# Performance work log

Hardware: AMD Instinct MI355X
Metric: run time of the kernel (lower is better)

The kernel has to match this reference:

```python
import jax, jax.numpy as jnp
import numpy as np


def setup_inputs() -> dict:
    key = jax.random.key(0)
    k1, k2 = jax.random.split(key)
    B, T, D, K = 16, 1024, 256, 8192
    x = jax.random.normal(k1, (B, T, D), dtype=jnp.float32)
    # mimic nn.Embedding init uniform_(-1/K, 1/K)
    codebook = jax.random.uniform(k2, (K, D), dtype=jnp.float32,
                                  minval=-1.0 / K, maxval=1.0 / K)
    return {"x": x, "codebook": codebook}


def reference(x, codebook):
    sg = jax.lax.stop_gradient
    x2 = jnp.sum(x * x, axis=-1, keepdims=True)               # [B, T, 1]
    c2 = jnp.sum(codebook * codebook, axis=-1)                # [K]
    xc = jnp.einsum('btd,kd->btk', x, codebook)               # [B, T, K]
    dist2 = x2 - 2.0 * xc + c2                                # [B, T, K]
    indices = jnp.argmin(dist2, axis=-1)                      # [B, T] int
    cb_vecs = codebook[indices]                               # [B, T, D]
    # straight-through estimator
    quantized = x + sg(cb_vecs - x)
    codebook_loss = jnp.mean((quantized - sg(x)) ** 2)
    commitment_loss = jnp.mean((sg(quantized) - x) ** 2)
    quantize_loss = codebook_loss + commitment_loss
    return (quantized, indices, quantize_loss)
```

## Files before the change

### kernel.cpp

```cpp
#include <hip/hip_runtime.h>
#include <float.h>

typedef __attribute__((ext_vector_type(8))) short short8;
typedef __attribute__((ext_vector_type(4))) float f32x4;

#define BT    16384
#define DM    256
#define KC    8192
#define QOFF  (BT * DM)
#define LOFF  (QOFF + BT)
#define MARGIN 2e-4f

#define E_XH 0
#define E_CH (BT * DM)
#define WS_BF16_BYTES ((size_t)(BT * DM + KC * DM) * 2)
#define WS_SLOT_OFF   WS_BF16_BYTES
#define WS_SLOT_BYTES ((size_t)64 * BT * 8)
#define WS_LP_OFF     (WS_SLOT_OFF + WS_SLOT_BYTES)
#define WS_NEED       (WS_LP_OFF + 4096 * 4)


__device__ inline ushort bf16rne(float f) {
    unsigned u = __float_as_uint(f);
    return (ushort)((u + 0x7FFFu + ((u >> 16) & 1u)) >> 16);
}
__device__ inline unsigned umax2(unsigned a, unsigned b) { return a > b ? a : b; }
__device__ inline unsigned umin2(unsigned a, unsigned b) { return a < b ? a : b; }

__device__ __forceinline__ void gl_lds16(const void* g, void* l) {
    __builtin_amdgcn_global_load_lds(
        (const __attribute__((address_space(1))) void*)g,
        (__attribute__((address_space(3))) void*)l, 16, 0, 0);
}

__global__ __launch_bounds__(256) void k_cvt(const float* __restrict__ x,
                                             const float* __restrict__ cb,
                                             ushort* __restrict__ ws) {
    const int XN = BT * DM / 4;
    const int CN = KC * DM / 4;
    int idx = blockIdx.x * 256 + threadIdx.x;
    const float4* src;
    ushort* dh; int o;
    if (idx < XN) { src = (const float4*)x; dh = ws + E_XH; o = idx; }
    else {
        o = idx - XN;
        if (o >= CN) return;
        src = (const float4*)cb; dh = ws + E_CH;
    }
    float4 v = src[o];
    ushort4 h;
    h.x = bf16rne(v.x);
    h.y = bf16rne(v.y);
    h.z = bf16rne(v.z);
    h.w = bf16rne(v.w);
    ((ushort4*)dh)[o] = h;
}

__global__ __launch_bounds__(512, 4) void k_main_mfma(const ushort* __restrict__ ws,
                                                      uint2* __restrict__ slotb) {
    __shared__ ushort sTok[2][64 * 256];
    __shared__ uint2  msc[2][4][64];

    const int tid = threadIdx.x;
    const int w = tid >> 6, L = tid & 63;
    const int lq = L >> 4, lr = L & 15;
    const int wm = w >> 1, wn = w & 1;
    const int grp   = blockIdx.x >> 3;
    const int chunk = blockIdx.x & 7;
    const int c0    = grp * 128 + wm * 32;
    const int tok0  = chunk * 2048;
    const unsigned lw = ((unsigned)wm << 5) | ((unsigned)lq << 2);

    const short8* ch8 = (const short8*)(ws + E_CH);
    const uint4*  xh4 = (const uint4*)(ws + E_XH);

    short8 a[2][8];
    #pragma unroll
    for (int i = 0; i < 2; ++i)
        #pragma unroll
        for (int ks = 0; ks < 8; ++ks)
            a[i][ks] = ch8[(size_t)(c0 + i * 16 + lr) * 32 + ks * 4 + lq];

    const int half = L >> 5;
    const int g32  = L & 31;

    {
        const uint4* src = xh4 + (size_t)(tok0 + w * 8) * 32;
        #pragma unroll
        for (int q = 0; q < 4; ++q) {
            int rrel = 2 * q + half;
            gl_lds16(src + (size_t)rrel * 32 + (g32 ^ (rrel & 7)),
                     &sTok[0][(w * 8 + 2 * q) * 256]);
        }
    }
    __syncthreads();

    uint2 mb0, mb1, mb2, mb3;

    auto emit = [&](uint2 mv, int pp) {
        slotb[(size_t)grp * BT + tok0 + pp * 64 + L] = mv;
    };

    for (int t = 0; t < 8; ++t) {
        #pragma unroll
        for (int pi = 0; pi < 4; ++pi) {
            const int p   = t * 4 + pi;
            const int cur = pi & 1;

            if (t < 7 || pi < 3) {
                const uint4* src = xh4 + (size_t)(tok0 + (p + 1) * 64 + w * 8) * 32;
                #pragma unroll
                for (int q = 0; q < 4; ++q) {
                    int rrel = 2 * q + half;
                    gl_lds16(src + (size_t)rrel * 32 + (g32 ^ (rrel & 7)),
                             &sTok[cur ^ 1][(w * 8 + 2 * q) * 256]);
                }
            }

            f32x4 acc[2][2];
            #pragma unroll
            for (int i = 0; i < 2; ++i)
                #pragma unroll
                for (int j = 0; j < 2; ++j)
                    acc[i][j] = (f32x4){0.25f, 0.25f, 0.25f, 0.25f};

            const ushort* tb = &sTok[cur][0];
            __builtin_amdgcn_s_setprio(1);
            #pragma unroll
            for (int ks = 0; ks < 8; ++ks) {
                short8 b[2];
                #pragma unroll
                for (int j = 0; j < 2; ++j) {
                    int row = wn * 32 + j * 16 + lr;
                    b[j] = *(const short8*)(tb + row * 256 + (((ks * 4 + lq) ^ (lr & 7)) * 8));
                }
                #pragma unroll
                for (int i = 0; i < 2; ++i)
                    #pragma unroll
                    for (int j = 0; j < 2; ++j)
                        acc[i][j] = __builtin_amdgcn_mfma_f32_16x16x32_bf16(a[i][ks], b[j], acc[i][j], 0, 0, 0);
            }
            __builtin_amdgcn_s_setprio(0);

            #pragma unroll
            for (int j = 0; j < 2; ++j) {
                unsigned h[4], l[4];
                #pragma unroll
                for (int i = 0; i < 2; ++i)
                    #pragma unroll
                    for (int rp = 0; rp < 2; ++rp) {
                        unsigned e0 = (__float_as_uint(acc[i][j][2 * rp])     & 0xFFFFFF80u) | lw | (i << 4) | (2 * rp);
                        unsigned e1 = (__float_as_uint(acc[i][j][2 * rp + 1]) & 0xFFFFFF80u) | lw | (i << 4) | (2 * rp + 1);
                        h[i * 2 + rp] = umax2(e0, e1);
                        l[i * 2 + rp] = umin2(e0, e1);
                    }
                unsigned ha = umax2(h[0], h[2]);
                unsigned la = umax2(umin2(h[0], h[2]), umax2(l[0], l[2]));
                unsigned hb = umax2(h[1], h[3]);
                unsigned lb = umax2(umin2(h[1], h[3]), umax2(l[1], l[3]));
                unsigned H  = umax2(ha, hb);
                unsigned L2 = umax2(umin2(ha, hb), umax2(la, lb));
                #pragma unroll
                for (int off = 16; off <= 32; off <<= 1) {
                    unsigned oH = (unsigned)__shfl_xor((int)H, off);
                    unsigned oL = (unsigned)__shfl_xor((int)L2, off);
                    unsigned m = umin2(H, oH);
                    H  = umax2(H, oH);
                    L2 = umax2(m, umax2(L2, oL));
                }
                if (lq == 0)
                    msc[cur][wm][wn * 32 + j * 16 + lr] = make_uint2(H, L2);
            }

            if (w == 0 && (t > 0 || pi > 0)) {
                const int pcur = cur ^ 1;
                uint2 m0 = msc[pcur][0][L];
                uint2 m1 = msc[pcur][1][L];
                uint2 m2 = msc[pcur][2][L];
                uint2 m3 = msc[pcur][3][L];
                unsigned H01 = umax2(m0.x, m1.x);
                unsigned l01 = umax2(umin2(m0.x, m1.x), umax2(m0.y, m1.y));
                unsigned H23 = umax2(m2.x, m3.x);
                unsigned l23 = umax2(umin2(m2.x, m3.x), umax2(m2.y, m3.y));
                unsigned H  = umax2(H01, H23);
                unsigned L2 = umax2(umin2(H01, H23), umax2(l01, l23));
                uint2 mm = make_uint2(H, L2);
                if (pi == 1)      mb0 = mm;
                else if (pi == 2) mb1 = mm;
                else if (pi == 3) mb2 = mm;
                else {
                    mb3 = mm;
                    int base = (t - 1) * 4;
                    emit(mb0, base);
                    emit(mb1, base + 1);
                    emit(mb2, base + 2);
                    emit(mb3, base + 3);
                }
            }

            __syncthreads();
        }
    }

    if (w == 0) {
        uint2 m0 = msc[1][0][L];
        uint2 m1 = msc[1][1][L];
        uint2 m2 = msc[1][2][L];
        uint2 m3 = msc[1][3][L];
        unsigned H01 = umax2(m0.x, m1.x);
        unsigned l01 = umax2(umin2(m0.x, m1.x), umax2(m0.y, m1.y));
        unsigned H23 = umax2(m2.x, m3.x);
        unsigned l23 = umax2(umin2(m2.x, m3.x), umax2(m2.y, m3.y));
        unsigned H  = umax2(H01, H23);
        unsigned L2 = umax2(umin2(H01, H23), umax2(l01, l23));
        emit(mb0, 28);
        emit(mb1, 29);
        emit(mb2, 30);
        emit(make_uint2(H, L2), 31);
    }
}

__global__ __launch_bounds__(256) void k_gather(const float* __restrict__ x,
                                                const float* __restrict__ cb,
                                                const uint2* __restrict__ slotb,
                                                float* __restrict__ out,
                                                float* __restrict__ lp) {
    __shared__ float4 xls[4][64];
    __shared__ int candk[4][16];
    __shared__ float bsum[4];

    const int w = threadIdx.x >> 6;
    const int L = threadIdx.x & 63;
    const int t = blockIdx.x * 4 + w;

    const float4 xv = ((const float4*)x)[(size_t)t * 64 + L];
    xls[w][L] = xv;

    const uint2 s = slotb[(size_t)L * BT + t];
    float v1 = __uint_as_float(s.x & 0xFFFFFF80u);
    float v2 = __uint_as_float(s.y & 0xFFFFFF80u);
    int   k1 = L * 128 + (int)(s.x & 127u);
    int   k2 = L * 128 + (int)(s.y & 127u);

    float lm = v1; int lk = k1;
    #pragma unroll
    for (int off = 32; off; off >>= 1) {
        float ov = __shfl_xor(lm, off);
        int   ok = __shfl_xor(lk, off);
        if (ov > lm || (ov == lm && ok < lk)) { lm = ov; lk = ok; }
    }
    const float thr = lm - MARGIN;

    int* ct = candk[w];
    if (L == 0) ct[0] = lk;
    int ncand = 1;
    #pragma unroll
    for (int ph = 0; ph < 2; ++ph) {
        float vv = ph ? v2 : v1;
        int   kf = ph ? k2 : k1;
        unsigned long long bal = __ballot(vv >= thr);
        while (bal) {
            int src = __ffsll(bal) - 1;
            bal &= bal - 1;
            int kv = __shfl(kf, src);
            if (L == 0 && ncand < 16) ct[ncand] = kv;
            ncand++;
        }
    }
    if (ncand > 16) ncand = 16;

    int best;
    if (ncand <= 1) {
        best = lk;
    } else {
        double dl = (double)xv.x * xv.x + (double)xv.y * xv.y
                  + (double)xv.z * xv.z + (double)xv.w * xv.w;
        #pragma unroll
        for (int off = 32; off; off >>= 1) dl += __shfl_xor(dl, off);
        const float x2 = (float)dl;

        const int g = L >> 2, l4 = L & 3;
        float sex = FLT_MAX;
        int   kk  = 0x7fffffff;
        if (g < ncand) {
            kk = ct[g];
            const float* xr = (const float*)&xls[w][0];
            const float* cr = cb + (size_t)kk * DM;
            float acc = 0.f;
            {
#pragma clang fp contract(off)
                #pragma unroll 8
                for (int m = 0; m < 64; m++) {
                    float p2 = xr[4 * m + l4] * cr[4 * m + l4];
                    acc = acc + p2;
                }
            }
            float t1 = acc + __shfl_xor(acc, 1);
            float xc = t1 + __shfl_xor(t1, 2);
            sex = x2 - 2.0f * xc;
        }
        #pragma unroll
        for (int off = 32; off; off >>= 1) {
            float os = __shfl_xor(sex, off);
            int   ok = __shfl_xor(kk, off);
            if (os < sex || (os == sex && ok < kk)) { sex = os; kk = ok; }
        }
        best = kk;
    }

    const float4 cv = ((const float4*)cb)[(size_t)best * 64 + L];
    float4 e, q;
    e.x = cv.x - xv.x; q.x = xv.x + e.x;
    e.y = cv.y - xv.y; q.y = xv.y + e.y;
    e.z = cv.z - xv.z; q.z = xv.z + e.z;
    e.w = cv.w - xv.w; q.w = xv.w + e.w;
    ((float4*)out)[(size_t)t * 64 + L] = q;
    if (L == 0) out[QOFF + t] = (float)best;

    float ls = e.x * e.x + e.y * e.y + e.z * e.z + e.w * e.w;
    #pragma unroll
    for (int off = 32; off; off >>= 1) ls += __shfl_xor(ls, off);
    if (L == 0) bsum[w] = ls;
    __syncthreads();
    if (threadIdx.x == 0)
        lp[blockIdx.x] = bsum[0] + bsum[1] + bsum[2] + bsum[3];
}


#define TM    64
#define TK    64
#define NSPLIT 2
#define KPS   (KC / NSPLIT)
#define LDSW  68

__global__ __launch_bounds__(256, 2) void k_main_f32(const float* __restrict__ x,
                                                     const float* __restrict__ cb,
                                                     float* __restrict__ out) {
    __shared__ float xs[TM * LDSW];
    __shared__ float cs[TK * LDSW];

    const int tid = threadIdx.x;
    const int ty = tid >> 4, tx = tid & 15;
    const int split = blockIdx.x & 1;
    const int tb    = blockIdx.x >> 1;
    const int t0    = tb * TM;
    const int kb0   = split * KPS;
    const int txc   = tx & 7;
    const int srow = tid >> 4;
    const int sc4  = tid & 15;
    const float4* x4  = (const float4*)x;
    const float4* cb4 = (const float4*)cb;

    float mv[4][4];
    int   mi[4][4];
    #pragma unroll
    for (int i = 0; i < 4; i++)
        #pragma unroll
        for (int j = 0; j < 4; j++) { mv[i][j] = -FLT_MAX; mi[i][j] = 0; }

    for (int k0 = 0; k0 < KPS; k0 += TK) {
        float dot[4][4];
        #pragma unroll
        for (int i = 0; i < 4; i++)
            #pragma unroll
            for (int j = 0; j < 4; j++) dot[i][j] = 0.f;

        for (int d0 = 0; d0 < DM; d0 += 64) {
            __syncthreads();
            const int d04 = d0 >> 2;
            #pragma unroll
            for (int r = 0; r < 4; r++) {
                int row = srow + 16 * r;
                float4 xv = x4[(size_t)(t0 + row) * 64 + d04 + sc4];
                *(float4*)&xs[row * LDSW + sc4 * 4] = xv;
                int gc = sc4 ^ ((row >> 2) & 7);
                float4 cv = cb4[(size_t)(kb0 + k0 + row) * 64 + d04 + gc];
                *(float4*)&cs[row * LDSW + sc4 * 4] = cv;
            }
            __syncthreads();

            #pragma unroll
            for (int u = 0; u < 16; u++) {
                float4 xa[4];
                #pragma unroll
                for (int i = 0; i < 4; i++)
                    xa[i] = *(const float4*)&xs[(ty * 4 + i) * LDSW + u * 4];
                const int ww = u ^ txc;
                float4 cv[4];
                #pragma unroll
                for (int j = 0; j < 4; j++)
                    cv[j] = *(const float4*)&cs[(tx * 4 + j) * LDSW + ww * 4];
                #pragma unroll
                for (int i = 0; i < 4; i++)
                    #pragma unroll
                    for (int j = 0; j < 4; j++) {
                        dot[i][j] = fmaf(xa[i].x, cv[j].x, dot[i][j]);
                        dot[i][j] = fmaf(xa[i].y, cv[j].y, dot[i][j]);
                        dot[i][j] = fmaf(xa[i].z, cv[j].z, dot[i][j]);
                        dot[i][j] = fmaf(xa[i].w, cv[j].w, dot[i][j]);
                    }
            }
        }

        const int kk0 = kb0 + k0 + tx * 4;
        #pragma unroll
        for (int i = 0; i < 4; i++)
            #pragma unroll
            for (int j = 0; j < 4; j++) {
                float d = dot[i][j];
                int   kk = kk0 + j;
                if (d > mv[i][3]) {
                    if (d > mv[i][1]) {
                        if (d > mv[i][0]) {
                            mv[i][3]=mv[i][2]; mi[i][3]=mi[i][2];
                            mv[i][2]=mv[i][1]; mi[i][2]=mi[i][1];
                            mv[i][1]=mv[i][0]; mi[i][1]=mi[i][0];
                            mv[i][0]=d;        mi[i][0]=kk;
                        } else {
                            mv[i][3]=mv[i][2]; mi[i][3]=mi[i][2];
                            mv[i][2]=mv[i][1]; mi[i][2]=mi[i][1];
                            mv[i][1]=d;        mi[i][1]=kk;
                        }
                    } else {
                        if (d > mv[i][2]) {
                            mv[i][3]=mv[i][2]; mi[i][3]=mi[i][2];
                            mv[i][2]=d;        mi[i][2]=kk;
                        } else {
                            mv[i][3]=d;        mi[i][3]=kk;
                        }
                    }
                }
            }
    }

    #pragma unroll
    for (int i = 0; i < 4; i++) {
        int t = t0 + ty * 4 + i;
        float4 v4 = { mv[i][0], mv[i][1], mv[i][2], mv[i][3] };
        float4 k4 = { (float)mi[i][0], (float)mi[i][1], (float)mi[i][2], (float)mi[i][3] };
        float4* dst = (float4*)(out + (size_t)t * DM + (split * 16 + tx) * 8);
        dst[0] = v4;
        dst[1] = k4;
    }
}

__global__ __launch_bounds__(256) void k_gather_f32(const float* __restrict__ x,
                                                    const float* __restrict__ cb,
                                                    float* __restrict__ out,
                                                    float* __restrict__ lp) {
    __shared__ float4 xls[4][64];
    __shared__ int candk[4][20];
    __shared__ float bsum[4];

    const int w = threadIdx.x >> 6;
    const int L = threadIdx.x & 63;
    const int t = blockIdx.x * 4 + w;

    const float4 xv = ((const float4*)x)[(size_t)t * 64 + L];
    xls[w][L] = xv;
    const float4 f = ((const float4*)(out + (size_t)t * DM))[L];
    const bool even = ((L & 1) == 0);

    double dl = (double)xv.x * xv.x + (double)xv.y * xv.y
              + (double)xv.z * xv.z + (double)xv.w * xv.w;
    #pragma unroll
    for (int off = 32; off; off >>= 1) dl += __shfl_xor(dl, off);
    const float x2 = (float)dl;

    float lm = even ? fmaxf(fmaxf(f.x, f.y), fmaxf(f.z, f.w)) : -FLT_MAX;
    #pragma unroll
    for (int off = 32; off; off >>= 1) lm = fmaxf(lm, __shfl_xor(lm, off));
    const float thr = lm - 5e-5f;

    int ncand = 0;
    #pragma unroll
    for (int j = 0; j < 4; j++) {
        float vj = (j == 0) ? f.x : (j == 1) ? f.y : (j == 2) ? f.z : f.w;
        bool flag = even && (vj >= thr);
        unsigned long long bal = __ballot(flag);
        while (bal) {
            int src = __ffsll(bal) - 1;
            bal &= bal - 1;
            float kv = __shfl(vj, src + 1);
            if (L == 0 && ncand < 20) candk[w][ncand] = (int)kv;
            ncand++;
        }
    }
    if (ncand > 16) ncand = 16;

    int best;
    if (ncand == 1) {
        best = candk[w][0];
    } else {
        const int g = L >> 2, l4 = L & 3;
        float sex = FLT_MAX;
        int   kk  = 0x7fffffff;
        if (g < ncand) {
            kk = candk[w][g];
            const float* xr = (const float*)&xls[w][0];
            const float* cr = cb + (size_t)kk * DM;
            float acc = 0.f;
            {
#pragma clang fp contract(off)
                #pragma unroll 8
                for (int m = 0; m < 64; m++) {
                    float p = xr[4 * m + l4] * cr[4 * m + l4];
                    acc = acc + p;
                }
            }
            float t1 = acc + __shfl_xor(acc, 1);
            float xc = t1 + __shfl_xor(t1, 2);
            sex = x2 - 2.0f * xc;
        }
        #pragma unroll
        for (int off = 32; off; off >>= 1) {
            float os = __shfl_xor(sex, off);
            int   ok = __shfl_xor(kk, off);
            if (os < sex || (os == sex && ok < kk)) { sex = os; kk = ok; }
        }
        best = kk;
    }

    const float4 cv = ((const float4*)cb)[(size_t)best * 64 + L];
    float4 e, q;
    e.x = cv.x - xv.x; q.x = xv.x + e.x;
    e.y = cv.y - xv.y; q.y = xv.y + e.y;
    e.z = cv.z - xv.z; q.z = xv.z + e.z;
    e.w = cv.w - xv.w; q.w = xv.w + e.w;
    ((float4*)out)[(size_t)t * 64 + L] = q;
    if (L == 0) out[QOFF + t] = (float)best;

    float ls = e.x * e.x + e.y * e.y + e.z * e.z + e.w * e.w;
    #pragma unroll
    for (int off = 32; off; off >>= 1) ls += __shfl_xor(ls, off);
    if (L == 0) bsum[w] = ls;
    __syncthreads();
    if (threadIdx.x == 0)
        lp[blockIdx.x] = bsum[0] + bsum[1] + bsum[2] + bsum[3];
}

__global__ __launch_bounds__(256) void k_loss(const float* __restrict__ lp,
                                              float* __restrict__ out) {
    __shared__ double sd[256];
    double s = 0.0;
    for (int i = threadIdx.x; i < BT / 4; i += 256) s += (double)lp[i];
    sd[threadIdx.x] = s;
    __syncthreads();
    for (int st = 128; st; st >>= 1) {
        if (threadIdx.x < st) sd[threadIdx.x] += sd[threadIdx.x + st];
        __syncthreads();
    }
    if (threadIdx.x == 0)
        out[LOFF] = (float)(2.0 * sd[0] / (double)QOFF);
}

extern "C" void kernel_launch(void* const* d_in, const int* in_sizes, int n_in,
                              void* d_out, int out_size, void* d_ws, size_t ws_size,
                              hipStream_t stream) {
    const float* x  = (const float*)d_in[0];
    const float* cb = (const float*)d_in[1];
    float* out = (float*)d_out;

    if (ws_size >= (size_t)WS_NEED) {
        ushort* wsu   = (ushort*)d_ws;
        uint2*  slotb = (uint2*)((char*)d_ws + WS_SLOT_OFF);
        float*  lp    = (float*)((char*)d_ws + WS_LP_OFF);
        k_cvt      <<<6144, 256, 0, stream>>>(x, cb, wsu);
        k_main_mfma<<<512,  512, 0, stream>>>(wsu, slotb);
        k_gather   <<<BT / 4, 256, 0, stream>>>(x, cb, slotb, out, lp);
        k_loss     <<<1,    256, 0, stream>>>(lp, out);
    } else {
        float* lp = (float*)d_ws;
        k_main_f32  <<<(BT / TM) * NSPLIT, 256, 0, stream>>>(x, cb, out);
        k_gather_f32<<<BT / 4,             256, 0, stream>>>(x, cb, out, lp);
        k_loss      <<<1,                  256, 0, stream>>>(lp, out);
    }
}
```

Measured before the change: 117.5 us.

## Restructure MFMA distance kernel into single-wave blocks holding tokens in registers

The main bf16 MFMA kernel now uses 64-thread blocks, each keeping 64 tokens in registers and streaming 1024 codes through double-buffered LDS panels of 16 codes. Each block keeps running top-2 packed keys per token across 8 panels, then writes one slot entry per group of 128 codes. This removes the multi-wave cross-wave reduction through shared memory and the __syncthreads in the inner loop. The trade-off is lower MFMA reuse per LDS load (one A fragment for four B) and a full vmcnt(0) wait every panel, which may expose global-to-LDS latency.

```diff
diff --git a/kernel.cpp b/kernel.cpp
--- a/kernel.cpp
+++ b/kernel.cpp
@@ -56,167 +56,111 @@
     ((ushort4*)dh)[o] = h;
 }
 
-__global__ __launch_bounds__(512, 4) void k_main_mfma(const ushort* __restrict__ ws,
-                                                      uint2* __restrict__ slotb) {
-    __shared__ ushort sTok[2][64 * 256];
-    __shared__ uint2  msc[2][4][64];
-
-    const int tid = threadIdx.x;
-    const int w = tid >> 6, L = tid & 63;
+__global__ __launch_bounds__(64, 2) void k_main_mfma(const ushort* __restrict__ ws,
+                                                     uint2* __restrict__ slotb) {
+    __shared__ ushort sCod[2][16 * 256];
+
+    const int L  = threadIdx.x;
     const int lq = L >> 4, lr = L & 15;
-    const int wm = w >> 1, wn = w & 1;
-    const int grp   = blockIdx.x >> 3;
-    const int chunk = blockIdx.x & 7;
-    const int c0    = grp * 128 + wm * 32;
-    const int tok0  = chunk * 2048;
-    const unsigned lw = ((unsigned)wm << 5) | ((unsigned)lq << 2);
-
-    const short8* ch8 = (const short8*)(ws + E_CH);
-    const uint4*  xh4 = (const uint4*)(ws + E_XH);
-
-    short8 a[2][8];
-    #pragma unroll
-    for (int i = 0; i < 2; ++i)
+    const int split = blockIdx.x & 7;
+    const int tt    = blockIdx.x >> 3;
+    const int t0    = tt * 64;
+    const int c0    = split * 1024;
+    const unsigned idlq = (unsigned)lq << 2;
+
+    const short8* xh8 = (const short8*)(ws + E_XH);
+    const uint4*  ch4 = (const uint4*)(ws + E_CH);
+
+    short8 b[4][8];
+    #pragma unroll
+    for (int j = 0; j < 4; ++j)
         #pragma unroll
         for (int ks = 0; ks < 8; ++ks)
-            a[i][ks] = ch8[(size_t)(c0 + i * 16 + lr) * 32 + ks * 4 + lq];
+            b[j][ks] = xh8[(size_t)(t0 + j * 16 + lr) * 32 + ks * 4 + lq];
 
     const int half = L >> 5;
     const int g32  = L & 31;
 
     {
-        const uint4* src = xh4 + (size_t)(tok0 + w * 8) * 32;
-        #pragma unroll
-        for (int q = 0; q < 4; ++q) {
+        const uint4* src = ch4 + (size_t)c0 * 32;
+        #pragma unroll
+        for (int q = 0; q < 8; ++q) {
             int rrel = 2 * q + half;
             gl_lds16(src + (size_t)rrel * 32 + (g32 ^ (rrel & 7)),
-                     &sTok[0][(w * 8 + 2 * q) * 256]);
-        }
-    }
-    __syncthreads();
-
-    uint2 mb0, mb1, mb2, mb3;
-
-    auto emit = [&](uint2 mv, int pp) {
-        slotb[(size_t)grp * BT + tok0 + pp * 64 + L] = mv;
-    };
-
-    for (int t = 0; t < 8; ++t) {
-        #pragma unroll
-        for (int pi = 0; pi < 4; ++pi) {
-            const int p   = t * 4 + pi;
-            const int cur = pi & 1;
-
-            if (t < 7 || pi < 3) {
-                const uint4* src = xh4 + (size_t)(tok0 + (p + 1) * 64 + w * 8) * 32;
+                     &sCod[0][q * 512]);
+        }
+    }
+    asm volatile("s_waitcnt vmcnt(0)" ::: "memory");
+    __builtin_amdgcn_sched_barrier(0);
+
+    for (int g = 0; g < 8; ++g) {
+        unsigned Hk[4], Lk[4];
+        #pragma unroll
+        for (int j = 0; j < 4; ++j) { Hk[j] = 0u; Lk[j] = 0u; }
+
+        #pragma unroll
+        for (int p = 0; p < 8; ++p) {
+            const int panel = g * 8 + p;
+            const int buf   = panel & 1;
+
+            if (panel < 63) {
+                const uint4* src = ch4 + (size_t)(c0 + (panel + 1) * 16) * 32;
                 #pragma unroll
-                for (int q = 0; q < 4; ++q) {
+                for (int q = 0; q < 8; ++q) {
                     int rrel = 2 * q + half;
                     gl_lds16(src + (size_t)rrel * 32 + (g32 ^ (rrel & 7)),
-                             &sTok[cur ^ 1][(w * 8 + 2 * q) * 256]);
+                             &sCod[buf ^ 1][q * 512]);
                 }
             }
 
-            f32x4 acc[2][2];
-            #pragma unroll
-            for (int i = 0; i < 2; ++i)
+            f32x4 acc[4];
+            #pragma unroll
+            for (int j = 0; j < 4; ++j)
+                acc[j] = (f32x4){0.25f, 0.25f, 0.25f, 0.25f};
+
+            const ushort* cbuf = &sCod[buf][0];
+            #pragma unroll
+            for (int ks = 0; ks < 8; ++ks) {
+                short8 a = *(const short8*)(cbuf + lr * 256 + (((ks * 4 + lq) ^ (lr & 7)) * 8));
                 #pragma unroll
-                for (int j = 0; j < 2; ++j)
-                    acc[i][j] = (f32x4){0.25f, 0.25f, 0.25f, 0.25f};
-
-            const ushort* tb = &sTok[cur][0];
-            __builtin_amdgcn_s_setprio(1);
-            #pragma unroll
-            for (int ks = 0; ks < 8; ++ks) {
-                short8 b[2];
-                #pragma unroll
-                for (int j = 0; j < 2; ++j) {
-                    int row = wn * 32 + j * 16 + lr;
-                    b[j] = *(const short8*)(tb + row * 256 + (((ks * 4 + lq) ^ (lr & 7)) * 8));
-                }
-                #pragma unroll
-                for (int i = 0; i < 2; ++i)
-                    #pragma unroll
-                    for (int j = 0; j < 2; ++j)
-                        acc[i][j] = __builtin_amdgcn_mfma_f32_16x16x32_bf16(a[i][ks], b[j], acc[i][j], 0, 0, 0);
-            }
-            __builtin_amdgcn_s_setprio(0);
-
-            #pragma unroll
-            for (int j = 0; j < 2; ++j) {
-                unsigned h[4], l[4];
-                #pragma unroll
-                for (int i = 0; i < 2; ++i)
-                    #pragma unroll
-                    for (int rp = 0; rp < 2; ++rp) {
-                        unsigned e0 = (__float_as_uint(acc[i][j][2 * rp])     & 0xFFFFFF80u) | lw | (i << 4) | (2 * rp);
-                        unsigned e1 = (__float_as_uint(acc[i][j][2 * rp + 1]) & 0xFFFFFF80u) | lw | (i << 4) | (2 * rp + 1);
-                        h[i * 2 + rp] = umax2(e0, e1);
-                        l[i * 2 + rp] = umin2(e0, e1);
-                    }
-                unsigned ha = umax2(h[0], h[2]);
-                unsigned la = umax2(umin2(h[0], h[2]), umax2(l[0], l[2]));
-                unsigned hb = umax2(h[1], h[3]);
-                unsigned lb = umax2(umin2(h[1], h[3]), umax2(l[1], l[3]));
-                unsigned H  = umax2(ha, hb);
-                unsigned L2 = umax2(umin2(ha, hb), umax2(la, lb));
-                #pragma unroll
-                for (int off = 16; off <= 32; off <<= 1) {
-                    unsigned oH = (unsigned)__shfl_xor((int)H, off);
-                    unsigned oL = (unsigned)__shfl_xor((int)L2, off);
-                    unsigned m = umin2(H, oH);
-                    H  = umax2(H, oH);
-                    L2 = umax2(m, umax2(L2, oL));
-                }
-                if (lq == 0)
-                    msc[cur][wm][wn * 32 + j * 16 + lr] = make_uint2(H, L2);
-            }
-
-            if (w == 0 && (t > 0 || pi > 0)) {
-                const int pcur = cur ^ 1;
-                uint2 m0 = msc[pcur][0][L];
-                uint2 m1 = msc[pcur][1][L];
-                uint2 m2 = msc[pcur][2][L];
-                uint2 m3 = msc[pcur][3][L];
-                unsigned H01 = umax2(m0.x, m1.x);
-                unsigned l01 = umax2(umin2(m0.x, m1.x), umax2(m0.y, m1.y));
-                unsigned H23 = umax2(m2.x, m3.x);
-                unsigned l23 = umax2(umin2(m2.x, m3.x), umax2(m2.y, m3.y));
-                unsigned H  = umax2(H01, H23);
-                unsigned L2 = umax2(umin2(H01, H23), umax2(l01, l23));
-                uint2 mm = make_uint2(H, L2);
-                if (pi == 1)      mb0 = mm;
-                else if (pi == 2) mb1 = mm;
-                else if (pi == 3) mb2 = mm;
-                else {
-                    mb3 = mm;
-                    int base = (t - 1) * 4;
-                    emit(mb0, base);
-                    emit(mb1, base + 1);
-                    emit(mb2, base + 2);
-                    emit(mb3, base + 3);
-                }
-            }
-
-            __syncthreads();
-        }
-    }
-
-    if (w == 0) {
-        uint2 m0 = msc[1][0][L];
-        uint2 m1 = msc[1][1][L];
-        uint2 m2 = msc[1][2][L];
-        uint2 m3 = msc[1][3][L];
-        unsigned H01 = umax2(m0.x, m1.x);
-        unsigned l01 = umax2(umin2(m0.x, m1.x), umax2(m0.y, m1.y));
-        unsigned H23 = umax2(m2.x, m3.x);
-        unsigned l23 = umax2(umin2(m2.x, m3.x), umax2(m2.y, m3.y));
-        unsigned H  = umax2(H01, H23);
-        unsigned L2 = umax2(umin2(H01, H23), umax2(l01, l23));
-        emit(mb0, 28);
-        emit(mb1, 29);
-        emit(mb2, 30);
-        emit(make_uint2(H, L2), 31);
+                for (int j = 0; j < 4; ++j)
+                    acc[j] = __builtin_amdgcn_mfma_f32_16x16x32_bf16(a, b[j][ks], acc[j], 0, 0, 0);
+            }
+
+            const unsigned idb = ((unsigned)p << 4) | idlq;
+            #pragma unroll
+            for (int j = 0; j < 4; ++j) {
+                unsigned e0 = (__float_as_uint(acc[j][0]) & 0xFFFFFF80u) | idb;
+                unsigned e1 = (__float_as_uint(acc[j][1]) & 0xFFFFFF80u) | idb | 1u;
+                unsigned e2 = (__float_as_uint(acc[j][2]) & 0xFFFFFF80u) | idb | 2u;
+                unsigned e3 = (__float_as_uint(acc[j][3]) & 0xFFFFFF80u) | idb | 3u;
+                unsigned h1 = umax2(e0, e1), l1 = umin2(e0, e1);
+                unsigned h2 = umax2(e2, e3), l2 = umin2(e2, e3);
+                unsigned hh = umax2(h1, h2);
+                unsigned hl = umax2(umin2(h1, h2), umax2(l1, l2));
+                unsigned nH = umax2(Hk[j], hh);
+                Lk[j] = umax2(umin2(Hk[j], hh), umax2(Lk[j], hl));
+                Hk[j] = nH;
+            }
+
+            asm volatile("s_waitcnt vmcnt(0)" ::: "memory");
+            __builtin_amdgcn_sched_barrier(0);
+        }
+
+        #pragma unroll
+        for (int j = 0; j < 4; ++j) {
+            unsigned H = Hk[j], Lo = Lk[j];
+            #pragma unroll
+            for (int off = 16; off <= 32; off <<= 1) {
+                unsigned oH = (unsigned)__shfl_xor((int)H, off);
+                unsigned oL = (unsigned)__shfl_xor((int)Lo, off);
+                unsigned m = umin2(H, oH);
+                H  = umax2(H, oH);
+                Lo = umax2(m, umax2(Lo, oL));
+            }
+            if (L < 16)
+                slotb[(size_t)(split * 8 + g) * BT + t0 + j * 16 + lr] = make_uint2(H, Lo);
+        }
     }
 }
 
@@ -566,7 +510,7 @@
         uint2*  slotb = (uint2*)((char*)d_ws + WS_SLOT_OFF);
         float*  lp    = (float*)((char*)d_ws + WS_LP_OFF);
         k_cvt      <<<6144, 256, 0, stream>>>(x, cb, wsu);
-        k_main_mfma<<<512,  512, 0, stream>>>(wsu, slotb);
+        k_main_mfma<<<2048, 64,  0, stream>>>(wsu, slotb);
         k_gather   <<<BT / 4, 256, 0, stream>>>(x, cb, slotb, out, lp);
         k_loss     <<<1,    256, 0, stream>>>(lp, out);
     } else {
```

Result: slower. 153.3 us (+30.5%).
